# Kernel tuning notes

Measured on AMD Instinct MI355X. Metric: run time of the kernel, lower is better.

## Reference

```python
import jax, jax.numpy as jnp
import numpy as np

N_ENT = 15000  # entity id range; also used for relation ids in this synthetic setup

def _triple_key(h, r, t):
    # Unique int64 key per (h, r, t) triple; max ~15000^3 < 2^63.
    return (h * N_ENT + r) * N_ENT + t

def setup_inputs() -> dict:
    key = jax.random.key(0)
    k1, k2, k3, k4 = jax.random.split(key, 4)
    Q, N = 100000, 10000000
    heads = jax.random.randint(k1, (Q,), 0, N_ENT, dtype=jnp.int64)
    rels = jax.random.randint(k2, (Q,), 0, N_ENT, dtype=jnp.int64)
    tails = jax.random.randint(k3, (Q,), 0, N_ENT, dtype=jnp.int64)
    data = jax.random.randint(k4, (3, N), 0, N_ENT, dtype=jnp.int64)
    return {"heads": heads, "rels": rels, "tails": tails, "data": data}

def reference(heads, rels, tails, data) -> jnp.ndarray:
    # Faithful to PerfeCT.forward: response[i] = 1 iff (heads[i], rels[i], tails[i])
    # appears as a row of data.T; output = 10 * (response - 0.5).
    data_keys = jnp.sort(_triple_key(data[0], data[1], data[2]))  # [N]
    q_keys = _triple_key(heads, rels, tails)                       # [Q]
    idx = jnp.searchsorted(data_keys, q_keys)
    idx = jnp.clip(idx, 0, data_keys.shape[0] - 1)
    member = (data_keys[idx] == q_keys).astype(jnp.float32)        # [Q]
    return 10.0 * (member - 0.5)
```

## Files before the change

### kernel.cpp

```cpp
#include <hip/hip_runtime.h>
#include <stdint.h>


typedef int iv4 __attribute__((ext_vector_type(4)));

#define EMPTY 0xFFFFFFFFu
#define BWORDS 32768

static __device__ __forceinline__ uint32_t mix32(uint32_t x) {
    x ^= x >> 16; x *= 0x85ebca6bu;
    x ^= x >> 13; x *= 0xc2b2ae35u;
    x ^= x >> 16;
    return x;
}
static __device__ __forceinline__ uint32_t hash2(uint32_t x) {
    return mix32(x ^ 0x9E3779B9u);
}
static __device__ __forceinline__ uint32_t key32(int h, int r, int t) {
    return ((uint32_t)h * 15000u + (uint32_t)r) * 15000u + (uint32_t)t;
}
static __device__ __forceinline__ void bloom_wm(uint32_t key, uint32_t* w, uint32_t* m) {
    uint32_t z = mix32(key);
    *w = z & (BWORDS - 1u);
    *m = (1u << ((z >> 15) & 31u)) | (1u << ((z >> 20) & 31u));
}

__global__ void k_zero(uint32_t* __restrict__ p, int zeroWords, int totalWords) {
    int stride = gridDim.x * blockDim.x;
    for (int i = blockIdx.x * blockDim.x + threadIdx.x; i < totalWords; i += stride)
        p[i] = (i < zeroWords) ? 0u : EMPTY;
}

__global__ void k_insert(const int* __restrict__ qh, const int* __restrict__ qr,
                         const int* __restrict__ qt,
                         uint32_t* __restrict__ bloom, uint32_t* __restrict__ keys,
                         uint32_t tmask, int Q) {
    int i = blockIdx.x * blockDim.x + threadIdx.x;
    if (i >= Q) return;
    uint32_t key = key32(qh[i], qr[i], qt[i]);
    if (key == EMPTY) return;
    uint32_t w, m; bloom_wm(key, &w, &m);
    atomicOr(&bloom[w], m);
    uint32_t slot = hash2(key) & tmask;
    while (true) {
        uint32_t prev = atomicCAS(&keys[slot], EMPTY, key);
        if (prev == EMPTY || prev == key) return;
        slot = (slot + 1) & tmask;
    }
}

static __device__ __forceinline__ void probe_mark(uint32_t key,
                                                  const uint32_t* __restrict__ keys,
                                                  uint32_t* __restrict__ flagbits,
                                                  uint32_t tmask) {
    uint32_t slot = hash2(key) & tmask;
    while (true) {
        uint32_t v = keys[slot];
        if (v == key) { atomicOr(&flagbits[slot >> 5], 1u << (slot & 31)); return; }
        if (v == EMPTY) return;
        slot = (slot + 1) & tmask;
    }
}

__global__ __launch_bounds__(1024) void k_scan(
        const int* __restrict__ dh, const int* __restrict__ dr,
        const int* __restrict__ dt,
        const uint32_t* __restrict__ bloom,
        const uint32_t* __restrict__ keys,
        uint32_t* __restrict__ flagbits, uint32_t* __restrict__ sent,
        uint32_t tmask, int nquad, int N) {
    __shared__ uint32_t lb[BWORDS];
    for (int i = threadIdx.x; i < BWORDS; i += 1024) lb[i] = bloom[i];
    __syncthreads();

    int stride = gridDim.x * blockDim.x;
    for (int j = blockIdx.x * blockDim.x + threadIdx.x; j < nquad; j += stride) {
        iv4 h4 = ((const iv4*)dh)[j];
        iv4 r4 = ((const iv4*)dr)[j];
        iv4 t4 = ((const iv4*)dt)[j];
        uint32_t k0 = key32(h4.x, r4.x, t4.x);
        uint32_t k1 = key32(h4.y, r4.y, t4.y);
        uint32_t k2 = key32(h4.z, r4.z, t4.z);
        uint32_t k3 = key32(h4.w, r4.w, t4.w);
        uint32_t w0, m0, w1, m1, w2, m2, w3, m3;
        bloom_wm(k0, &w0, &m0); bloom_wm(k1, &w1, &m1);
        bloom_wm(k2, &w2, &m2); bloom_wm(k3, &w3, &m3);
        uint32_t v0 = lb[w0], v1 = lb[w1], v2 = lb[w2], v3 = lb[w3];
        if (k0 == EMPTY) *sent = 1u; else if ((v0 & m0) == m0) probe_mark(k0, keys, flagbits, tmask);
        if (k1 == EMPTY) *sent = 1u; else if ((v1 & m1) == m1) probe_mark(k1, keys, flagbits, tmask);
        if (k2 == EMPTY) *sent = 1u; else if ((v2 & m2) == m2) probe_mark(k2, keys, flagbits, tmask);
        if (k3 == EMPTY) *sent = 1u; else if ((v3 & m3) == m3) probe_mark(k3, keys, flagbits, tmask);
    }
    int tail = N & 3;
    if (tail && blockIdx.x == 0 && threadIdx.x < (unsigned)tail) {
        int j = N - 1 - (int)threadIdx.x;
        uint32_t k = key32(dh[j], dr[j], dt[j]);
        if (k == EMPTY) *sent = 1u;
        else probe_mark(k, keys, flagbits, tmask);
    }
}

__global__ void k_out(const int* __restrict__ qh, const int* __restrict__ qr,
                      const int* __restrict__ qt,
                      const uint32_t* __restrict__ keys,
                      const uint32_t* __restrict__ flagbits,
                      const uint32_t* __restrict__ sent,
                      float* __restrict__ out, uint32_t tmask, int Q) {
    int i = blockIdx.x * blockDim.x + threadIdx.x;
    if (i >= Q) return;
    uint32_t key = key32(qh[i], qr[i], qt[i]);
    float v = -5.0f;
    if (key == EMPTY) {
        v = (*sent) ? 5.0f : -5.0f;
    } else {
        uint32_t slot = hash2(key) & tmask;
        while (true) {
            uint32_t kv = keys[slot];
            if (kv == key) { v = ((flagbits[slot >> 5] >> (slot & 31)) & 1u) ? 5.0f : -5.0f; break; }
            if (kv == EMPTY) break;
            slot = (slot + 1) & tmask;
        }
    }
    out[i] = v;
}

extern "C" void kernel_launch(void* const* d_in, const int* in_sizes, int n_in,
                              void* d_out, int out_size, void* d_ws, size_t ws_size,
                              hipStream_t stream) {
    const int* qh = (const int*)d_in[0];
    const int* qr = (const int*)d_in[1];
    const int* qt = (const int*)d_in[2];
    const int* data = (const int*)d_in[3];
    int Q = in_sizes[0];
    int N = in_sizes[3] / 3;
    const int* dh = data;
    const int* dr = data + (size_t)N;
    const int* dt = data + 2 * (size_t)N;
    float* out = (float*)d_out;

    int tb = 18;
    size_t bloomB = (size_t)BWORDS * 4;
    size_t need = bloomB + ((size_t)1 << (tb - 3)) + 256 + ((size_t)4 << tb);
    if (need > ws_size) tb = 17;
    size_t flagB = (size_t)1 << (tb - 3);
    uint32_t tmask = ((uint32_t)1 << tb) - 1u;

    uint32_t* bloom    = (uint32_t*)d_ws;
    uint32_t* flagbits = (uint32_t*)((char*)d_ws + bloomB);
    uint32_t* sent     = (uint32_t*)((char*)d_ws + bloomB + flagB);
    uint32_t* keys     = (uint32_t*)((char*)d_ws + bloomB + flagB + 256);

    int zeroWords  = (int)((bloomB + flagB + 256) / 4);
    int totalWords = zeroWords + (1 << tb);
    k_zero<<<1024, 256, 0, stream>>>((uint32_t*)d_ws, zeroWords, totalWords);

    int qblocks = (Q + 255) / 256;
    k_insert<<<qblocks, 256, 0, stream>>>(qh, qr, qt, bloom, keys, tmask, Q);

    int nquad = N / 4;
    k_scan<<<256, 1024, 0, stream>>>(dh, dr, dt, bloom, keys, flagbits, sent,
                                     tmask, nquad, N);

    k_out<<<qblocks, 256, 0, stream>>>(qh, qr, qt, keys, flagbits, sent, out, tmask, Q);
}
```

Baseline: 235.8 us.

## Defer hash-table probes for Bloom hits to end of scan, process eight keys per thread

Each scan thread now handles eight triples per iteration, two 16-byte loads from separate halves of the array. Keys that pass the Bloom filter are no longer probed inline. They go into a per-thread shared-memory queue of up to six entries, or into a global overflow buffer drained by a new k_probe kernel. The goal is to keep the streaming loop free of divergent dependent global loads so memory-level parallelism stays high. The cost is a global atomic counter on overflow, an extra kernel launch, more shared memory (which could lower occupancy), and workspace layout changes.

```diff
diff --git a/kernel.cpp b/kernel.cpp
--- a/kernel.cpp
+++ b/kernel.cpp
@@ -4,8 +4,10 @@
 
 typedef int iv4 __attribute__((ext_vector_type(4)));
 
-#define EMPTY 0xFFFFFFFFu
+#define EMPTY  0xFFFFFFFFu
 #define BWORDS 32768
+#define QSLOTS 6
+#define TPB    1024
 
 static __device__ __forceinline__ uint32_t mix32(uint32_t x) {
     x ^= x >> 16; x *= 0x85ebca6bu;
@@ -62,42 +64,81 @@
     }
 }
 
-__global__ __launch_bounds__(1024) void k_scan(
+static __device__ __forceinline__ void ovf_push(uint32_t key,
+                                                uint32_t* __restrict__ ovf_cnt,
+                                                uint32_t* __restrict__ ovf, uint32_t ovfcap,
+                                                const uint32_t* __restrict__ keys,
+                                                uint32_t* __restrict__ flagbits, uint32_t tmask) {
+    uint32_t idx = atomicAdd(ovf_cnt, 1u);
+    if (idx < ovfcap) ovf[idx] = key;
+    else probe_mark(key, keys, flagbits, tmask);
+}
+
+__global__ __launch_bounds__(TPB) void k_scan(
         const int* __restrict__ dh, const int* __restrict__ dr,
         const int* __restrict__ dt,
         const uint32_t* __restrict__ bloom,
         const uint32_t* __restrict__ keys,
         uint32_t* __restrict__ flagbits, uint32_t* __restrict__ sent,
-        uint32_t tmask, int nquad, int N) {
+        uint32_t* __restrict__ ovf_cnt, uint32_t* __restrict__ ovf, uint32_t ovfcap,
+        uint32_t tmask, int noct, int N) {
     __shared__ uint32_t lb[BWORDS];
-    for (int i = threadIdx.x; i < BWORDS; i += 1024) lb[i] = bloom[i];
+    __shared__ uint32_t qb[TPB * QSLOTS];
+    for (int i = threadIdx.x; i < BWORDS; i += TPB) lb[i] = bloom[i];
     __syncthreads();
 
+    const iv4* H = (const iv4*)dh;
+    const iv4* R = (const iv4*)dr;
+    const iv4* T = (const iv4*)dt;
+    int cnt = 0;
     int stride = gridDim.x * blockDim.x;
-    for (int j = blockIdx.x * blockDim.x + threadIdx.x; j < nquad; j += stride) {
-        iv4 h4 = ((const iv4*)dh)[j];
-        iv4 r4 = ((const iv4*)dr)[j];
-        iv4 t4 = ((const iv4*)dt)[j];
-        uint32_t k0 = key32(h4.x, r4.x, t4.x);
-        uint32_t k1 = key32(h4.y, r4.y, t4.y);
-        uint32_t k2 = key32(h4.z, r4.z, t4.z);
-        uint32_t k3 = key32(h4.w, r4.w, t4.w);
-        uint32_t w0, m0, w1, m1, w2, m2, w3, m3;
-        bloom_wm(k0, &w0, &m0); bloom_wm(k1, &w1, &m1);
-        bloom_wm(k2, &w2, &m2); bloom_wm(k3, &w3, &m3);
+
+#define TESTQ(kk, vv, mm)                                                          \
+    if ((kk) == EMPTY) *sent = 1u;                                                 \
+    else if (((vv) & (mm)) == (mm)) {                                              \
+        if (cnt < QSLOTS) qb[cnt * TPB + threadIdx.x] = (kk);                      \
+        else ovf_push((kk), ovf_cnt, ovf, ovfcap, keys, flagbits, tmask);          \
+        cnt++;                                                                     \
+    }
+
+    for (int j = blockIdx.x * blockDim.x + threadIdx.x; j < noct; j += stride) {
+        iv4 hA = H[j], rA = R[j], tA = T[j];
+        iv4 hB = H[j + noct], rB = R[j + noct], tB = T[j + noct];
+        uint32_t k0 = key32(hA.x, rA.x, tA.x), k1 = key32(hA.y, rA.y, tA.y);
+        uint32_t k2 = key32(hA.z, rA.z, tA.z), k3 = key32(hA.w, rA.w, tA.w);
+        uint32_t k4 = key32(hB.x, rB.x, tB.x), k5 = key32(hB.y, rB.y, tB.y);
+        uint32_t k6 = key32(hB.z, rB.z, tB.z), k7 = key32(hB.w, rB.w, tB.w);
+        uint32_t w0,m0,w1,m1,w2,m2,w3,m3,w4,m4,w5,m5,w6,m6,w7,m7;
+        bloom_wm(k0,&w0,&m0); bloom_wm(k1,&w1,&m1); bloom_wm(k2,&w2,&m2); bloom_wm(k3,&w3,&m3);
+        bloom_wm(k4,&w4,&m4); bloom_wm(k5,&w5,&m5); bloom_wm(k6,&w6,&m6); bloom_wm(k7,&w7,&m7);
         uint32_t v0 = lb[w0], v1 = lb[w1], v2 = lb[w2], v3 = lb[w3];
-        if (k0 == EMPTY) *sent = 1u; else if ((v0 & m0) == m0) probe_mark(k0, keys, flagbits, tmask);
-        if (k1 == EMPTY) *sent = 1u; else if ((v1 & m1) == m1) probe_mark(k1, keys, flagbits, tmask);
-        if (k2 == EMPTY) *sent = 1u; else if ((v2 & m2) == m2) probe_mark(k2, keys, flagbits, tmask);
-        if (k3 == EMPTY) *sent = 1u; else if ((v3 & m3) == m3) probe_mark(k3, keys, flagbits, tmask);
-    }
-    int tail = N & 3;
-    if (tail && blockIdx.x == 0 && threadIdx.x < (unsigned)tail) {
-        int j = N - 1 - (int)threadIdx.x;
+        uint32_t v4 = lb[w4], v5 = lb[w5], v6 = lb[w6], v7 = lb[w7];
+        TESTQ(k0, v0, m0) TESTQ(k1, v1, m1) TESTQ(k2, v2, m2) TESTQ(k3, v3, m3)
+        TESTQ(k4, v4, m4) TESTQ(k5, v5, m5) TESTQ(k6, v6, m6) TESTQ(k7, v7, m7)
+    }
+#undef TESTQ
+
+    int rem = N - 8 * noct;
+    if (blockIdx.x == 0 && (int)threadIdx.x < rem) {
+        int j = 8 * noct + threadIdx.x;
         uint32_t k = key32(dh[j], dr[j], dt[j]);
         if (k == EMPTY) *sent = 1u;
         else probe_mark(k, keys, flagbits, tmask);
     }
+
+    int m = cnt < QSLOTS ? cnt : QSLOTS;
+    for (int c = 0; c < m; ++c)
+        probe_mark(qb[c * TPB + threadIdx.x], keys, flagbits, tmask);
+}
+
+__global__ void k_probe(const uint32_t* __restrict__ ovf,
+                        const uint32_t* __restrict__ ovf_cnt, uint32_t ovfcap,
+                        const uint32_t* __restrict__ keys,
+                        uint32_t* __restrict__ flagbits, uint32_t tmask) {
+    uint32_t n = *ovf_cnt; if (n > ovfcap) n = ovfcap;
+    int stride = gridDim.x * blockDim.x;
+    for (uint32_t i = blockIdx.x * blockDim.x + threadIdx.x; i < n; i += stride)
+        probe_mark(ovf[i], keys, flagbits, tmask);
 }
 
 __global__ void k_out(const int* __restrict__ qh, const int* __restrict__ qr,
@@ -139,16 +180,20 @@
     float* out = (float*)d_out;
 
     int tb = 18;
+    uint32_t ovfcap = 65536;
     size_t bloomB = (size_t)BWORDS * 4;
-    size_t need = bloomB + ((size_t)1 << (tb - 3)) + 256 + ((size_t)4 << tb);
-    if (need > ws_size) tb = 17;
+    size_t need = bloomB + ((size_t)1 << (tb - 3)) + 256 + ((size_t)4 << tb) + 4ull * ovfcap;
+    if (need > ws_size) { ovfcap = 8192;
+        need = bloomB + ((size_t)1 << (tb - 3)) + 256 + ((size_t)4 << tb) + 4ull * ovfcap; }
+    if (need > ws_size) { tb = 17; }
     size_t flagB = (size_t)1 << (tb - 3);
     uint32_t tmask = ((uint32_t)1 << tb) - 1u;
 
     uint32_t* bloom    = (uint32_t*)d_ws;
     uint32_t* flagbits = (uint32_t*)((char*)d_ws + bloomB);
-    uint32_t* sent     = (uint32_t*)((char*)d_ws + bloomB + flagB);
+    uint32_t* hdr      = (uint32_t*)((char*)d_ws + bloomB + flagB);
     uint32_t* keys     = (uint32_t*)((char*)d_ws + bloomB + flagB + 256);
+    uint32_t* ovf      = (uint32_t*)((char*)d_ws + bloomB + flagB + 256 + ((size_t)4 << tb));
 
     int zeroWords  = (int)((bloomB + flagB + 256) / 4);
     int totalWords = zeroWords + (1 << tb);
@@ -157,9 +202,11 @@
     int qblocks = (Q + 255) / 256;
     k_insert<<<qblocks, 256, 0, stream>>>(qh, qr, qt, bloom, keys, tmask, Q);
 
-    int nquad = N / 4;
-    k_scan<<<256, 1024, 0, stream>>>(dh, dr, dt, bloom, keys, flagbits, sent,
-                                     tmask, nquad, N);
-
-    k_out<<<qblocks, 256, 0, stream>>>(qh, qr, qt, keys, flagbits, sent, out, tmask, Q);
-}
+    int noct = N / 8;
+    k_scan<<<256, TPB, 0, stream>>>(dh, dr, dt, bloom, keys, flagbits,
+                                    hdr, hdr + 1, ovf, ovfcap, tmask, noct, N);
+
+    k_probe<<<64, 256, 0, stream>>>(ovf, hdr + 1, ovfcap, keys, flagbits, tmask);
+
+    k_out<<<qblocks, 256, 0, stream>>>(qh, qr, qt, keys, flagbits, hdr, out, tmask, Q);
+}
```

Result: faster. 220.0 us (-6.7%).
